# Optimization experiments

Hardware: AMD Instinct MI355X
Metric: run time of the kernel (lower is better)

The kernel has to match this reference:

```python
import jax, jax.numpy as jnp
import numpy as np
from jax import lax

A = 3          # anchors per scale
C = 80         # num foreground classes (COCO)
NMS_THRESH = 0.45
NMS_TOPK = 400
POST_NMS = 100


def setup_inputs() -> dict:
    key = jax.random.key(0)
    k0, k1, k2 = jax.random.split(key, 3)
    B = 8
    ch = A * (C + 5)  # 255
    # raw head outputs (pre-decode conv activations), modest scale so exp() stays sane
    tip0 = jax.random.normal(k0, (B, ch, 19, 19), jnp.float32) * 0.5
    tip1 = jax.random.normal(k1, (B, ch, 38, 38), jnp.float32) * 0.5
    tip2 = jax.random.normal(k2, (B, ch, 76, 76), jnp.float32) * 0.5
    # standard YOLOv3 COCO anchors, deepest scale (stride 32) first
    anchors0 = jnp.array([[116., 90.], [156., 198.], [373., 326.]], jnp.float32)
    anchors1 = jnp.array([[30., 61.], [62., 45.], [59., 119.]], jnp.float32)
    anchors2 = jnp.array([[10., 13.], [16., 30.], [33., 23.]], jnp.float32)
    return dict(tip0=tip0, tip1=tip1, tip2=tip2,
                anchors0=anchors0, anchors1=anchors1, anchors2=anchors2)


def _decode(tip, anchors, stride):
    """YOLOOutputV3 inference decode. tip: (B, A*(C+5), H, W)."""
    B, _, H, W = tip.shape
    # (B, A*(C+5), H*W) -> (B, H*W, A, C+5)
    pred = tip.reshape(B, A * (C + 5), H * W).transpose(0, 2, 1).reshape(B, H * W, A, C + 5)
    gx, gy = jnp.meshgrid(jnp.arange(W), jnp.arange(H))       # each (H, W)
    offsets = jnp.stack([gx, gy], -1).reshape(1, H * W, 1, 2).astype(tip.dtype)
    centers = (jax.nn.sigmoid(pred[..., :2]) + offsets) * stride          # (B,HW,A,2)
    scales = jnp.exp(pred[..., 2:4]) * anchors.reshape(1, 1, A, 2)        # (B,HW,A,2)
    conf = jax.nn.sigmoid(pred[..., 4:5])                                 # objectness
    cls_scores = jax.nn.sigmoid(pred[..., 5:]) * conf                      # (B,HW,A,C)
    wh = scales * 0.5
    bbox = jnp.concatenate([centers - wh, centers + wh], -1)               # corner format
    return bbox.reshape(B, H * W * A, 4), cls_scores.reshape(B, H * W * A, C)


def _pairwise_iou(b):
    """b: (K,4) corner boxes -> (K,K) IoU."""
    x1, y1, x2, y2 = b[:, 0], b[:, 1], b[:, 2], b[:, 3]
    area = jnp.maximum(x2 - x1, 0.) * jnp.maximum(y2 - y1, 0.)
    iw = jnp.maximum(jnp.minimum(x2[:, None], x2[None, :]) - jnp.maximum(x1[:, None], x1[None, :]), 0.)
    ih = jnp.maximum(jnp.minimum(y2[:, None], y2[None, :]) - jnp.maximum(y1[:, None], y1[None, :]), 0.)
    inter = iw * ih
    return inter / (area[:, None] + area[None, :] - inter + 1e-12)


def _nms_single(det):
    """Class-aware greedy NMS on one image. det: (M,6) = (cid, score, x1,y1,x2,y2)."""
    K = NMS_TOPK
    _, idx = lax.top_k(det[:, 1], K)     # sort by score, keep top K
    d = det[idx]                          # (K,6), descending score
    iou = _pairwise_iou(d[:, 2:6])
    same = d[:, 0][:, None] == d[:, 0][None, :]   # only same class suppresses
    valid = d[:, 1] > 0.
    rng = jnp.arange(K)

    def body(i, keep):
        sup = (iou[i] > NMS_THRESH) & same[i] & (rng > i) & keep[i] & valid[i]
        return keep & ~sup

    keep = lax.fori_loop(0, K, body, jnp.ones((K,), bool)) & valid
    d = jnp.where(keep[:, None], d, jnp.full_like(d, -1.))
    order = jnp.argsort(-d[:, 1])         # kept (sorted) first, suppressed (-1) last
    return d[order][:POST_NMS]            # (POST_NMS, 6)


def _detect(tip0, tip1, tip2, anchors0, anchors1, anchors2):
    dets = []
    for tip, anc, stride in ((tip0, anchors0, 32), (tip1, anchors1, 16), (tip2, anchors2, 8)):
        bbox, scores = _decode(tip, anc, stride)          # (B,N,4), (B,N,C)
        B, N, _ = bbox.shape
        ids = jnp.broadcast_to(jnp.arange(C, dtype=bbox.dtype)[None, None, :, None], (B, N, C, 1))
        sc = scores[..., None]                            # (B,N,C,1)
        bx = jnp.broadcast_to(bbox[:, :, None, :], (B, N, C, 4))
        dets.append(jnp.concatenate([ids, sc, bx], -1).reshape(B, N * C, 6))
    det = jnp.concatenate(dets, 1)                        # (B, M, 6)
    return jax.vmap(_nms_single)(det)                     # (B, POST_NMS, 6)


def reference(tip0, tip1, tip2, anchors0, anchors1, anchors2):
    res = _detect(tip0, tip1, tip2, anchors0, anchors1, anchors2)
    ids = res[..., 0:1]
    scores = res[..., 1:2]
    bboxes = res[..., 2:6]
    return ids, scores, bboxes
```

## Files before the change

### kernel.cpp

```cpp
#include <hip/hip_runtime.h>
#include <stdint.h>

#define NUMA 3
#define NUMC 80
#define CAP  49152
#define KTOP 400
#define POST 100
#define EQCAP 1024
#define PFCAP 2048
#define KEY0 0x3EE66666u
#define KEYTOP 0x3F800000u
#define LBUF 1024
#define NMASK (KTOP * 7)

typedef float f32x4 __attribute__((ext_vector_type(4)));

__device__ __forceinline__ float sigmoidf_(float x) { return 1.0f / (1.0f + expf(-x)); }
__device__ __forceinline__ unsigned uminu(unsigned a, unsigned b) { return a < b ? a : b; }

__global__ void init_kernel(unsigned* __restrict__ p) {
    int i = blockIdx.x * blockDim.x + threadIdx.x;
    if (i < 24) p[i] = 0;
}

__global__ __launch_bounds__(256) void score_main(
        const float* __restrict__ t0, const float* __restrict__ t1,
        const float* __restrict__ t2,
        unsigned* __restrict__ ccnt, unsigned* __restrict__ ckey,
        unsigned* __restrict__ cidx)
{
    __shared__ unsigned lkey[LBUF], lidx[LBUF];
    __shared__ unsigned lcnt, lbase;
    const int tid = threadIdx.x;
    if (tid == 0) lcnt = 0;
    __syncthreads();

    const int ba = blockIdx.z;
    const int b = ba / 3, a = ba - 3 * b;
    const int c0 = blockIdx.y * 10;
    const int cx = blockIdx.x;

    #define LEMIT(SC, IDX) do { \
        unsigned key_ = __float_as_uint(SC); \
        if (key_ >= KEY0) { \
            unsigned pos_ = atomicAdd(&lcnt, 1u); \
            if (pos_ < LBUF) { lkey[pos_] = key_; lidx[pos_] = (IDX); } \
        } \
    } while (0)

    if (cx < 2) {
        const int hw = cx * 256 + tid;
        if (hw < 361) {
            const float* base = t0 + (size_t)(b * 255 + a * 85) * 361;
            float cr = base[4 * 361 + hw];
            const float* p0 = base + (size_t)(5 + c0) * 361 + hw;
            float x0 = p0[0 * 361], x1 = p0[1 * 361], x2 = p0[2 * 361], x3 = p0[3 * 361];
            float x4 = p0[4 * 361], x5 = p0[5 * 361], x6 = p0[6 * 361], x7 = p0[7 * 361];
            float x8 = p0[8 * 361], x9 = p0[9 * 361];
            float cf = sigmoidf_(cr);
            unsigned ib = (unsigned)((hw * NUMA + a) * NUMC + c0);
            LEMIT(sigmoidf_(x0) * cf, ib + 0);
            LEMIT(sigmoidf_(x1) * cf, ib + 1);
            LEMIT(sigmoidf_(x2) * cf, ib + 2);
            LEMIT(sigmoidf_(x3) * cf, ib + 3);
            LEMIT(sigmoidf_(x4) * cf, ib + 4);
            LEMIT(sigmoidf_(x5) * cf, ib + 5);
            LEMIT(sigmoidf_(x6) * cf, ib + 6);
            LEMIT(sigmoidf_(x7) * cf, ib + 7);
            LEMIT(sigmoidf_(x8) * cf, ib + 8);
            LEMIT(sigmoidf_(x9) * cf, ib + 9);
        }
    } else {
        const float* tip; int vHW, v, candOff;
        if (cx < 4) { tip = t1; vHW = 361;  v = (cx - 2) * 256 + tid; candOff = 86640; }
        else        { tip = t2; vHW = 1444; v = (cx - 4) * 256 + tid; candOff = 433200; }
        if (v < vHW) {
            const f32x4* bp = (const f32x4*)(tip + (size_t)(b * 255 + a * 85) * (size_t)(vHW * 4));
            f32x4 cv = bp[(size_t)4 * vHW + v];
            const f32x4* p0 = bp + (size_t)(5 + c0) * vHW + v;
            f32x4 s0 = p0[0 * (size_t)vHW], s1 = p0[1 * (size_t)vHW];
            f32x4 s2 = p0[2 * (size_t)vHW], s3 = p0[3 * (size_t)vHW];
            f32x4 s4 = p0[4 * (size_t)vHW], s5 = p0[5 * (size_t)vHW];
            f32x4 s6 = p0[6 * (size_t)vHW], s7 = p0[7 * (size_t)vHW];
            f32x4 s8 = p0[8 * (size_t)vHW], s9 = p0[9 * (size_t)vHW];
            float cf0 = sigmoidf_(cv[0]), cf1 = sigmoidf_(cv[1]);
            float cf2 = sigmoidf_(cv[2]), cf3 = sigmoidf_(cv[3]);
            unsigned ib0 = (unsigned)(candOff + (v * 4 * NUMA + a) * NUMC + c0);
            #define EMIT4(S, U) do { \
                unsigned ib = ib0 + (U); \
                LEMIT(sigmoidf_((S)[0]) * cf0, ib); \
                LEMIT(sigmoidf_((S)[1]) * cf1, ib + 240); \
                LEMIT(sigmoidf_((S)[2]) * cf2, ib + 480); \
                LEMIT(sigmoidf_((S)[3]) * cf3, ib + 720); \
            } while (0)
            EMIT4(s0, 0); EMIT4(s1, 1); EMIT4(s2, 2); EMIT4(s3, 3);
            EMIT4(s4, 4); EMIT4(s5, 5); EMIT4(s6, 6); EMIT4(s7, 7);
            EMIT4(s8, 8); EMIT4(s9, 9);
            #undef EMIT4
        }
    }
    #undef LEMIT

    __syncthreads();
    if (tid == 0) {
        unsigned c = lcnt;
        if (c > LBUF) {
            atomicOr(&ccnt[b], 0x80000000u);
            lbase = 0xFFFFFFFFu;
        } else {
            lbase = atomicAdd(&ccnt[b], c);
        }
    }
    __syncthreads();
    unsigned c = uminu(lcnt, (unsigned)LBUF);
    unsigned basep = lbase;
    if (basep != 0xFFFFFFFFu) {
        for (unsigned i = tid; i < c; i += 256) {
            unsigned p = basep + i;
            if (p < CAP) {
                ckey[(size_t)b * CAP + p] = lkey[i];
                cidx[(size_t)b * CAP + p] = lidx[i];
            }
        }
    }
}

__device__ __forceinline__ void wave_select(const unsigned* h, int nbins, unsigned rank,
                                            unsigned* resv, int tid)
{
    if (tid >= 64) return;
    const int lane = tid;
    const int cs = nbins >> 6;
    unsigned v = 0;
    for (int k = 0; k < cs; k++) {
        int off = (k + lane) & (cs - 1);
        v += h[lane * cs + off];
    }
    unsigned S = v;
    #pragma unroll
    for (int o = 1; o < 64; o <<= 1) {
        unsigned t = (unsigned)__shfl_down((int)S, o);
        if (lane + o < 64) S += t;
    }
    unsigned long long bm = __ballot(S >= rank);
    if (bm == 0ull) bm = 1ull;
    int C = 63 - __builtin_clzll(bm);
    unsigned SC = (unsigned)__builtin_amdgcn_readlane((int)S, C);
    unsigned vC = (unsigned)__builtin_amdgcn_readlane((int)v, C);
    unsigned rem = rank - (SC - vC);
    unsigned w = (lane < cs) ? h[C * cs + lane] : 0u;
    unsigned T = w;
    #pragma unroll
    for (int o = 1; o < 64; o <<= 1) {
        unsigned t = (unsigned)__shfl_down((int)T, o);
        if (lane + o < 64) T += t;
    }
    unsigned long long bm2 = __ballot((T >= rem) && (lane < cs));
    if (bm2 == 0ull) bm2 = 1ull;
    int B = 63 - __builtin_clzll(bm2);
    unsigned TB = (unsigned)__builtin_amdgcn_readlane((int)T, B);
    unsigned wB = (unsigned)__builtin_amdgcn_readlane((int)w, B);
    if (lane == 0) {
        resv[0] = (unsigned)(C * cs + B);
        resv[1] = rem - (TB - wB);
    }
}

__global__ __launch_bounds__(1024) void fb_all(
        const float* __restrict__ t0, const float* __restrict__ t1,
        const float* __restrict__ t2,
        unsigned* __restrict__ cutb, unsigned* __restrict__ ccnt,
        unsigned* __restrict__ flags,
        unsigned* __restrict__ ckey, unsigned* __restrict__ cidx)
{
    const int b = blockIdx.x;
    unsigned cc = ccnt[b];
    if (cc >= KTOP && cc <= CAP) return;

    __shared__ unsigned lh[2048];
    __shared__ unsigned resv[2];
    __shared__ unsigned fcnt;
    const int tid = threadIdx.x;
    const int NPOS = 3 * (361 + 1444 + 5776);

    for (int i = tid; i < 2048; i += 1024) lh[i] = 0;
    if (tid == 0) fcnt = 0;
    __syncthreads();

    for (int p = tid; p < NPOS; p += 1024) {
        const float* tip; int HW, pp;
        if (p < 1083)      { tip = t0; HW = 361;  pp = p; }
        else if (p < 5415) { tip = t1; HW = 1444; pp = p - 1083; }
        else               { tip = t2; HW = 5776; pp = p - 5415; }
        int a = pp / HW, hwl = pp - a * HW;
        const float* base = tip + (size_t)(b * 255 + a * 85) * HW;
        float cf = sigmoidf_(base[4 * HW + hwl]);
        for (int u = 0; u < NUMC; u++) {
            float sc = sigmoidf_(base[(size_t)(5 + u) * HW + hwl]) * cf;
            atomicAdd(&lh[__float_as_uint(sc) >> 19], 1u);
        }
    }
    __syncthreads();
    wave_select(lh, 2048, KTOP, resv, tid);
    __syncthreads();
    unsigned cutbin = resv[0];
    unsigned cutkey = cutbin << 19;
    __syncthreads();

    unsigned* ck = ckey + (size_t)b * CAP;
    unsigned* ci = cidx + (size_t)b * CAP;
    for (int p = tid; p < NPOS; p += 1024) {
        const float* tip; int HW, pp, candOff;
        if (p < 1083)      { tip = t0; HW = 361;  pp = p;        candOff = 0; }
        else if (p < 5415) { tip = t1; HW = 1444; pp = p - 1083; candOff = 86640; }
        else               { tip = t2; HW = 5776; pp = p - 5415; candOff = 433200; }
        int a = pp / HW, hwl = pp - a * HW;
        const float* base = tip + (size_t)(b * 255 + a * 85) * HW;
        float cf = sigmoidf_(base[4 * HW + hwl]);
        unsigned ib0 = (unsigned)(candOff + (hwl * NUMA + a) * NUMC);
        for (int u = 0; u < NUMC; u++) {
            float sc = sigmoidf_(base[(size_t)(5 + u) * HW + hwl]) * cf;
            unsigned key = __float_as_uint(sc);
            if (key >= cutkey) {
                unsigned pos = atomicAdd(&fcnt, 1u);
                if (pos < CAP) { ck[pos] = key; ci[pos] = ib0 + (unsigned)u; }
            }
        }
    }
    __syncthreads();
    if (tid == 0) { ccnt[b] = fcnt; cutb[b] = cutbin; flags[b] = 1u; }
}

__global__ __launch_bounds__(1024) void topk_nms(
        const float* __restrict__ t0, const float* __restrict__ t1,
        const float* __restrict__ t2,
        const float* __restrict__ anc0, const float* __restrict__ anc1,
        const float* __restrict__ anc2,
        const unsigned* __restrict__ ckey, const unsigned* __restrict__ cidx,
        const unsigned* __restrict__ ccnt, const unsigned* __restrict__ cutb,
        const unsigned* __restrict__ flags, float* __restrict__ out)
{
    const int b = blockIdx.x;
    const int tid = threadIdx.x;
    const int T = 1024;

    __shared__ unsigned long long poolq[4160];
    unsigned* hist = (unsigned*)poolq;
    unsigned* pk   = (unsigned*)poolq + 4096;
    unsigned* pi   = (unsigned*)poolq + 6144;
    unsigned long long* maskL = poolq;
    float* bx1 = (float*)(poolq + 2800);
    float* by1 = bx1 + 400;
    float* bx2 = by1 + 400;
    float* by2 = bx2 + 400;
    int*   bcid = (int*)(poolq + 3600);
    unsigned long long* vkeep = poolq + 3800;
    float* oid = (float*)(poolq + 3808);
    float* osc = oid + 100;
    float* obb = osc + 100;

    __shared__ unsigned selk[512], seli[512];
    __shared__ unsigned eqi[EQCAP];
    __shared__ unsigned resv[2];
    __shared__ unsigned cnts[3];

    const unsigned* ck = ckey + (size_t)b * CAP;
    const unsigned* ci = cidx + (size_t)b * CAP;
    unsigned n = uminu(ccnt[b], (unsigned)CAP);

    unsigned kbase = flags[b] ? (cutb[b] << 19) : KEY0;
    unsigned span = (KEYTOP - kbase) + 1u;
    unsigned SH = 0;
    while ((span >> SH) > 2047u) SH++;

    for (int i = tid; i < 2048; i += T) hist[i] = 0;
    __syncthreads();
    {
        unsigned n4 = n >> 2;
        const uint4* ck4 = (const uint4*)ck;
        for (unsigned i = tid; i < n4; i += T) {
            uint4 k = ck4[i];
            atomicAdd(&hist[(k.x - kbase) >> SH], 1u);
            atomicAdd(&hist[(k.y - kbase) >> SH], 1u);
            atomicAdd(&hist[(k.z - kbase) >> SH], 1u);
            atomicAdd(&hist[(k.w - kbase) >> SH], 1u);
        }
        for (unsigned i = (n4 << 2) + tid; i < n; i += T)
            atomicAdd(&hist[(ck[i] - kbase) >> SH], 1u);
    }
    __syncthreads();
    wave_select(hist, 2048, KTOP, resv, tid);
    __syncthreads();
    unsigned Bf = resv[0];
    __syncthreads();

    if (tid == 0) { cnts[0] = 0; cnts[1] = 0; cnts[2] = 0; }
    __syncthreads();
    for (unsigned i = tid; i < n; i += T) {
        unsigned k = ck[i];
        if (((k - kbase) >> SH) >= Bf) {
            unsigned q = atomicAdd(&cnts[2], 1u);
            if (q < (unsigned)PFCAP) { pk[q] = k; pi[q] = ci[i]; }
        }
    }
    __syncthreads();
    unsigned pfCnt = cnts[2];
    bool useP = (pfCnt <= (unsigned)PFCAP);
    unsigned m = useP ? pfCnt : n;

    for (int i = tid; i < 4096; i += T) hist[i] = 0;
    __syncthreads();
    for (unsigned i = tid; i < m; i += T) {
        unsigned k = useP ? pk[i] : ck[i];
        atomicAdd(&hist[k >> 19], 1u);
    }
    __syncthreads();
    wave_select(hist, 4096, KTOP, resv, tid);
    __syncthreads();
    unsigned b1 = resv[0], r2 = resv[1];
    __syncthreads();

    for (int i = tid; i < 4096; i += T) hist[i] = 0;
    __syncthreads();
    for (unsigned i = tid; i < m; i += T) {
        unsigned k = useP ? pk[i] : ck[i];
        if ((k >> 19) == b1) atomicAdd(&hist[(k >> 7) & 0xFFFu], 1u);
    }
    __syncthreads();
    wave_select(hist, 4096, r2, resv, tid);
    __syncthreads();
    unsigned b2 = resv[0], r3 = resv[1];
    __syncthreads();

    for (int i = tid; i < 128; i += T) hist[i] = 0;
    __syncthreads();
    unsigned pref = (b1 << 12) | b2;
    for (unsigned i = tid; i < m; i += T) {
        unsigned k = useP ? pk[i] : ck[i];
        if ((k >> 7) == pref) atomicAdd(&hist[k & 127u], 1u);
    }
    __syncthreads();
    wave_select(hist, 128, r3, resv, tid);
    __syncthreads();
    unsigned b3 = resv[0], needEq = resv[1];
    unsigned K400 = (b1 << 19) | (b2 << 7) | b3;
    __syncthreads();

    for (int i = tid; i < 512; i += T) { selk[i] = 0u; seli[i] = 0xFFFFFFFFu; }
    for (int i = tid; i < EQCAP; i += T) eqi[i] = 0xFFFFFFFFu;
    __syncthreads();
    for (unsigned i = tid; i < m; i += T) {
        unsigned k = useP ? pk[i] : ck[i];
        if (k > K400) {
            unsigned idx = useP ? pi[i] : ci[i];
            unsigned p = atomicAdd(&cnts[0], 1u);
            if (p < 512u) { selk[p] = k; seli[p] = idx; }
        } else if (k == K400) {
            unsigned idx = useP ? pi[i] : ci[i];
            unsigned q = atomicAdd(&cnts[1], 1u);
            if (q < (unsigned)EQCAP) eqi[q] = idx;
        }
    }
    __syncthreads();
    unsigned selCnt = uminu(cnts[0], (unsigned)KTOP);
    unsigned eqN   = uminu(cnts[1], (unsigned)EQCAP);

    if (eqN > needEq) {
        int P2 = 1; while ((unsigned)P2 < eqN) P2 <<= 1;
        for (int k2 = 2; k2 <= P2; k2 <<= 1) {
            for (int j = k2 >> 1; j > 0; j >>= 1) {
                __syncthreads();
                for (int i = tid; i < P2; i += T) {
                    int ixj = i ^ j;
                    if (ixj > i && ixj < P2) {
                        unsigned va = eqi[i], vb = eqi[ixj];
                        bool up = ((i & k2) == 0);
                        if (up ? (va > vb) : (va < vb)) { eqi[i] = vb; eqi[ixj] = va; }
                    }
                }
            }
        }
        __syncthreads();
    }
    for (unsigned t2v = tid; t2v < needEq; t2v += T) {
        unsigned p = selCnt + t2v;
        if (p < KTOP) { selk[p] = K400; seli[p] = eqi[t2v]; }
    }
    __syncthreads();

    for (int k2 = 2; k2 <= 512; k2 <<= 1) {
        int j = k2 >> 1;
        for (; j >= 64; j >>= 1) {
            __syncthreads();
            if (tid < 512) {
                int i = tid, ixj = i ^ j;
                if (ixj > i) {
                    unsigned ka = selk[i], kb = selk[ixj], ia = seli[i], ib = seli[ixj];
                    bool before = (ka > kb) || (ka == kb && ia < ib);
                    bool up = ((i & k2) == 0);
                    if (up ? !before : before) {
                        selk[i] = kb; selk[ixj] = ka; seli[i] = ib; seli[ixj] = ia;
                    }
                }
            }
        }
        __syncthreads();
        if (tid < 512) {
            for (; j > 0; j >>= 1) {
                int i = tid, ixj = i ^ j;
                if (ixj > i) {
                    unsigned ka = selk[i], kb = selk[ixj], ia = seli[i], ib = seli[ixj];
                    bool before = (ka > kb) || (ka == kb && ia < ib);
                    bool up = ((i & k2) == 0);
                    if (up ? !before : before) {
                        selk[i] = kb; selk[ixj] = ka; seli[i] = ib; seli[ixj] = ia;
                    }
                }
            }
        }
    }
    __syncthreads();

    if (tid < KTOP) {
        unsigned idx = seli[tid];
        if (idx == 0xFFFFFFFFu) {
            bx1[tid] = -1.f; by1[tid] = -1.f; bx2[tid] = -1.f; by2[tid] = -1.f;
            bcid[tid] = 0;
        } else {
            const float* tip; const float* anc; int HW, W, candOff; float strideF;
            if (idx < 86640u)       { tip = t0; anc = anc0; HW = 361;  W = 19; strideF = 32.f; candOff = 0; }
            else if (idx < 433200u) { tip = t1; anc = anc1; HW = 1444; W = 38; strideF = 16.f; candOff = 86640; }
            else                    { tip = t2; anc = anc2; HW = 5776; W = 76; strideF = 8.f;  candOff = 433200; }
            unsigned local = idx - (unsigned)candOff;
            int cls = (int)(local % NUMC);
            int nn  = (int)(local / NUMC);
            int a = nn % NUMA, hwl = nn / NUMA;
            const float* base = tip + (size_t)(b * 255 + a * 85) * HW + hwl;
            float tx = base[0];
            float ty = base[(size_t)HW];
            float tw = base[(size_t)2 * HW];
            float th = base[(size_t)3 * HW];
            float fx = (float)(hwl % W), fy = (float)(hwl / W);
            float cx = (sigmoidf_(tx) + fx) * strideF;
            float cy = (sigmoidf_(ty) + fy) * strideF;
            float hw_ = expf(tw) * anc[2 * a]     * 0.5f;
            float hh_ = expf(th) * anc[2 * a + 1] * 0.5f;
            bx1[tid] = cx - hw_; by1[tid] = cy - hh_;
            bx2[tid] = cx + hw_; by2[tid] = cy + hh_;
            bcid[tid] = cls;
        }
    }
    __syncthreads();

    for (int p = tid; p < NMASK; p += T) {
        int i = p / 7, w = p - i * 7;
        float x1i = bx1[i], y1i = by1[i], x2i = bx2[i], y2i = by2[i];
        float ai = fmaxf(x2i - x1i, 0.f) * fmaxf(y2i - y1i, 0.f);
        int cidI = bcid[i];
        unsigned long long mq = 0ull;
        int j0 = w * 64;
        int j1 = j0 + 64; if (j1 > KTOP) j1 = KTOP;
        int js = j0 > i + 1 ? j0 : i + 1;
        for (int j = js; j < j1; j++) {
            if (bcid[j] != cidI) continue;
            float iw = fminf(x2i, bx2[j]) - fmaxf(x1i, bx1[j]);
            float ih = fminf(y2i, by2[j]) - fmaxf(y1i, by1[j]);
            iw = fmaxf(iw, 0.f); ih = fmaxf(ih, 0.f);
            float inter = iw * ih;
            float aj = fmaxf(bx2[j] - bx1[j], 0.f) * fmaxf(by2[j] - by1[j], 0.f);
            float iou = inter / (ai + aj - inter + 1e-12f);
            if (iou > 0.45f) mq |= (1ull << (j - j0));
        }
        maskL[p] = mq;
    }
    __syncthreads();

    if (tid < 64) {
        const int lane = tid;
        unsigned long long keep = 0ull;
        if (lane < 7) keep = (lane == 6) ? 0xFFFFull : ~0ull;
        unsigned long long mb[8];
        #pragma unroll
        for (int k = 0; k < 8; k++)
            mb[k] = (lane < 7) ? maskL[k * 7 + lane] : 0ull;
        for (int ib = 0; ib < KTOP; ib += 8) {
            #pragma unroll
            for (int k = 0; k < 8; k++) {
                int i = ib + k;
                unsigned long long mq = mb[k];
                int nf = ib + 8 + k;
                mb[k] = (lane < 7 && nf < KTOP) ? maskL[nf * 7 + lane] : 0ull;
                int w = i >> 6;
                unsigned klo = (unsigned)__builtin_amdgcn_readlane((int)(unsigned)(keep & 0xFFFFFFFFull), w);
                unsigned khi = (unsigned)__builtin_amdgcn_readlane((int)(unsigned)(keep >> 32), w);
                unsigned long long kw = ((unsigned long long)khi << 32) | klo;
                if ((kw >> (i & 63)) & 1ull) keep &= ~mq;
            }
        }
        if (lane < 7) vkeep[lane] = keep;
    } else {
        int q = tid - 64;
        if (q < POST) { oid[q] = -1.f; osc[q] = -1.f; }
        if (q < POST * 4) obb[q] = -1.f;
    }
    __syncthreads();

    if (tid < KTOP) {
        int w = tid >> 6, bp = tid & 63;
        unsigned long long kw = vkeep[w];
        if ((kw >> bp) & 1ull) {
            int r = 0;
            for (int q = 0; q < w; q++) r += __popcll(vkeep[q]);
            r += __popcll(kw & ((1ull << bp) - 1ull));
            if (r < POST) {
                oid[r] = (float)bcid[tid];
                osc[r] = __uint_as_float(selk[tid]);
                obb[r * 4 + 0] = bx1[tid];
                obb[r * 4 + 1] = by1[tid];
                obb[r * 4 + 2] = bx2[tid];
                obb[r * 4 + 3] = by2[tid];
            }
        }
    }
    __syncthreads();
    if (tid < POST) {
        out[b * POST + tid]       = oid[tid];
        out[800 + b * POST + tid] = osc[tid];
    }
    if (tid < POST * 4) out[1600 + b * POST * 4 + tid] = obb[tid];
}

extern "C" void kernel_launch(void* const* d_in, const int* in_sizes, int n_in,
                              void* d_out, int out_size, void* d_ws, size_t ws_size,
                              hipStream_t stream)
{
    const float* tip0 = (const float*)d_in[0];
    const float* tip1 = (const float*)d_in[1];
    const float* tip2 = (const float*)d_in[2];
    const float* anc0 = (const float*)d_in[3];
    const float* anc1 = (const float*)d_in[4];
    const float* anc2 = (const float*)d_in[5];
    float* out = (float*)d_out;

    unsigned* cutb  = (unsigned*)d_ws;
    unsigned* ccnt  = cutb + 8;
    unsigned* flags = ccnt + 8;
    unsigned* ckey  = flags + 8;
    unsigned* cidx  = ckey + (size_t)8 * CAP;

    init_kernel<<<1, 64, 0, stream>>>(cutb);

    dim3 g(10, 8, 24);
    score_main<<<g, 256, 0, stream>>>(tip0, tip1, tip2, ccnt, ckey, cidx);
    fb_all<<<8, 1024, 0, stream>>>(tip0, tip1, tip2, cutb, ccnt, flags, ckey, cidx);
    topk_nms<<<8, 1024, 0, stream>>>(tip0, tip1, tip2, anc0, anc1, anc2,
                                     ckey, cidx, ccnt, cutb, flags, out);
}
```

Before: 198.9 us.

## Split top-k/NMS into select, parallel mask, and greedy kernels; prefilter logits

The monolithic per-batch topk_nms kernel is split into three kernels. topk_sel decodes boxes to global memory, mask_kernel computes the IoU masks across many blocks per batch, and greedy_kernel runs the serial suppression scan. The mask loop also rotates the j start per word to spread shared-memory accesses. Separately, score_main now compares raw logits against a threshold derived from objectness, so the sigmoid is skipped for candidates that cannot pass. The cost is two extra launches and round trips through global memory.

After: 191.3 us. 3.8% less time.

```diff
diff --git a/kernel.cpp b/kernel.cpp
--- a/kernel.cpp
+++ b/kernel.cpp
@@ -18,6 +18,13 @@
 __device__ __forceinline__ float sigmoidf_(float x) { return 1.0f / (1.0f + expf(-x)); }
 __device__ __forceinline__ unsigned uminu(unsigned a, unsigned b) { return a < b ? a : b; }
 
+__device__ __forceinline__ float thr_for(float cf) {
+    if (!(cf >= 0.45f)) return 3.0e38f;
+    float q = 0.449f / cf;
+    float r = q / (1.0f - q);
+    return logf(r) - 0.01f;
+}
+
 __global__ void init_kernel(unsigned* __restrict__ p) {
     int i = blockIdx.x * blockDim.x + threadIdx.x;
     if (i < 24) p[i] = 0;
@@ -58,17 +65,18 @@
             float x4 = p0[4 * 361], x5 = p0[5 * 361], x6 = p0[6 * 361], x7 = p0[7 * 361];
             float x8 = p0[8 * 361], x9 = p0[9 * 361];
             float cf = sigmoidf_(cr);
+            float xt = thr_for(cf);
             unsigned ib = (unsigned)((hw * NUMA + a) * NUMC + c0);
-            LEMIT(sigmoidf_(x0) * cf, ib + 0);
-            LEMIT(sigmoidf_(x1) * cf, ib + 1);
-            LEMIT(sigmoidf_(x2) * cf, ib + 2);
-            LEMIT(sigmoidf_(x3) * cf, ib + 3);
-            LEMIT(sigmoidf_(x4) * cf, ib + 4);
-            LEMIT(sigmoidf_(x5) * cf, ib + 5);
-            LEMIT(sigmoidf_(x6) * cf, ib + 6);
-            LEMIT(sigmoidf_(x7) * cf, ib + 7);
-            LEMIT(sigmoidf_(x8) * cf, ib + 8);
-            LEMIT(sigmoidf_(x9) * cf, ib + 9);
+            if (x0 > xt) LEMIT(sigmoidf_(x0) * cf, ib + 0);
+            if (x1 > xt) LEMIT(sigmoidf_(x1) * cf, ib + 1);
+            if (x2 > xt) LEMIT(sigmoidf_(x2) * cf, ib + 2);
+            if (x3 > xt) LEMIT(sigmoidf_(x3) * cf, ib + 3);
+            if (x4 > xt) LEMIT(sigmoidf_(x4) * cf, ib + 4);
+            if (x5 > xt) LEMIT(sigmoidf_(x5) * cf, ib + 5);
+            if (x6 > xt) LEMIT(sigmoidf_(x6) * cf, ib + 6);
+            if (x7 > xt) LEMIT(sigmoidf_(x7) * cf, ib + 7);
+            if (x8 > xt) LEMIT(sigmoidf_(x8) * cf, ib + 8);
+            if (x9 > xt) LEMIT(sigmoidf_(x9) * cf, ib + 9);
         }
     } else {
         const float* tip; int vHW, v, candOff;
@@ -85,13 +93,15 @@
             f32x4 s8 = p0[8 * (size_t)vHW], s9 = p0[9 * (size_t)vHW];
             float cf0 = sigmoidf_(cv[0]), cf1 = sigmoidf_(cv[1]);
             float cf2 = sigmoidf_(cv[2]), cf3 = sigmoidf_(cv[3]);
+            float xt0 = thr_for(cf0), xt1 = thr_for(cf1);
+            float xt2 = thr_for(cf2), xt3 = thr_for(cf3);
             unsigned ib0 = (unsigned)(candOff + (v * 4 * NUMA + a) * NUMC + c0);
             #define EMIT4(S, U) do { \
                 unsigned ib = ib0 + (U); \
-                LEMIT(sigmoidf_((S)[0]) * cf0, ib); \
-                LEMIT(sigmoidf_((S)[1]) * cf1, ib + 240); \
-                LEMIT(sigmoidf_((S)[2]) * cf2, ib + 480); \
-                LEMIT(sigmoidf_((S)[3]) * cf3, ib + 720); \
+                if ((S)[0] > xt0) LEMIT(sigmoidf_((S)[0]) * cf0, ib); \
+                if ((S)[1] > xt1) LEMIT(sigmoidf_((S)[1]) * cf1, ib + 240); \
+                if ((S)[2] > xt2) LEMIT(sigmoidf_((S)[2]) * cf2, ib + 480); \
+                if ((S)[3] > xt3) LEMIT(sigmoidf_((S)[3]) * cf3, ib + 720); \
             } while (0)
             EMIT4(s0, 0); EMIT4(s1, 1); EMIT4(s2, 2); EMIT4(s3, 3);
             EMIT4(s4, 4); EMIT4(s5, 5); EMIT4(s6, 6); EMIT4(s7, 7);
@@ -231,37 +241,27 @@
     if (tid == 0) { ccnt[b] = fcnt; cutb[b] = cutbin; flags[b] = 1u; }
 }
 
-__global__ __launch_bounds__(1024) void topk_nms(
+__global__ __launch_bounds__(1024) void topk_sel(
         const float* __restrict__ t0, const float* __restrict__ t1,
         const float* __restrict__ t2,
         const float* __restrict__ anc0, const float* __restrict__ anc1,
         const float* __restrict__ anc2,
         const unsigned* __restrict__ ckey, const unsigned* __restrict__ cidx,
         const unsigned* __restrict__ ccnt, const unsigned* __restrict__ cutb,
-        const unsigned* __restrict__ flags, float* __restrict__ out)
+        const unsigned* __restrict__ flags,
+        float* __restrict__ dX1, float* __restrict__ dY1,
+        float* __restrict__ dX2, float* __restrict__ dY2,
+        float* __restrict__ dSC, unsigned* __restrict__ dCID)
 {
     const int b = blockIdx.x;
     const int tid = threadIdx.x;
     const int T = 1024;
 
-    __shared__ unsigned long long poolq[4160];
-    unsigned* hist = (unsigned*)poolq;
-    unsigned* pk   = (unsigned*)poolq + 4096;
-    unsigned* pi   = (unsigned*)poolq + 6144;
-    unsigned long long* maskL = poolq;
-    float* bx1 = (float*)(poolq + 2800);
-    float* by1 = bx1 + 400;
-    float* bx2 = by1 + 400;
-    float* by2 = bx2 + 400;
-    int*   bcid = (int*)(poolq + 3600);
-    unsigned long long* vkeep = poolq + 3800;
-    float* oid = (float*)(poolq + 3808);
-    float* osc = oid + 100;
-    float* obb = osc + 100;
-
+    __shared__ unsigned hist[4096];
+    __shared__ unsigned resv[2];
     __shared__ unsigned selk[512], seli[512];
     __shared__ unsigned eqi[EQCAP];
-    __shared__ unsigned resv[2];
+    __shared__ unsigned pk[PFCAP], pi[PFCAP];
     __shared__ unsigned cnts[3];
 
     const unsigned* ck = ckey + (size_t)b * CAP;
@@ -423,9 +423,10 @@
 
     if (tid < KTOP) {
         unsigned idx = seli[tid];
+        int o = b * KTOP + tid;
         if (idx == 0xFFFFFFFFu) {
-            bx1[tid] = -1.f; by1[tid] = -1.f; bx2[tid] = -1.f; by2[tid] = -1.f;
-            bcid[tid] = 0;
+            dX1[o] = -1.f; dY1[o] = -1.f; dX2[o] = -1.f; dY2[o] = -1.f;
+            dSC[o] = __uint_as_float(selk[tid]); dCID[o] = 0u;
         } else {
             const float* tip; const float* anc; int HW, W, candOff; float strideF;
             if (idx < 86640u)       { tip = t0; anc = anc0; HW = 361;  W = 19; strideF = 32.f; candOff = 0; }
@@ -445,34 +446,70 @@
             float cy = (sigmoidf_(ty) + fy) * strideF;
             float hw_ = expf(tw) * anc[2 * a]     * 0.5f;
             float hh_ = expf(th) * anc[2 * a + 1] * 0.5f;
-            bx1[tid] = cx - hw_; by1[tid] = cy - hh_;
-            bx2[tid] = cx + hw_; by2[tid] = cy + hh_;
-            bcid[tid] = cls;
-        }
-    }
-    __syncthreads();
-
-    for (int p = tid; p < NMASK; p += T) {
+            dX1[o] = cx - hw_; dY1[o] = cy - hh_;
+            dX2[o] = cx + hw_; dY2[o] = cy + hh_;
+            dSC[o] = __uint_as_float(selk[tid]);
+            dCID[o] = (unsigned)cls;
+        }
+    }
+}
+
+__global__ __launch_bounds__(256) void mask_kernel(
+        const float* __restrict__ dX1, const float* __restrict__ dY1,
+        const float* __restrict__ dX2, const float* __restrict__ dY2,
+        const unsigned* __restrict__ dCID, unsigned long long* __restrict__ maskG)
+{
+    __shared__ float lx1[KTOP], ly1[KTOP], lx2[KTOP], ly2[KTOP];
+    __shared__ int lcid[KTOP];
+    const int b = blockIdx.y;
+    const int tid = threadIdx.x;
+    for (int i = tid; i < KTOP; i += 256) {
+        int o = b * KTOP + i;
+        lx1[i] = dX1[o]; ly1[i] = dY1[o];
+        lx2[i] = dX2[o]; ly2[i] = dY2[o];
+        lcid[i] = (int)dCID[o];
+    }
+    __syncthreads();
+    int p = blockIdx.x * 256 + tid;
+    if (p < NMASK) {
         int i = p / 7, w = p - i * 7;
-        float x1i = bx1[i], y1i = by1[i], x2i = bx2[i], y2i = by2[i];
+        float x1i = lx1[i], y1i = ly1[i], x2i = lx2[i], y2i = ly2[i];
         float ai = fmaxf(x2i - x1i, 0.f) * fmaxf(y2i - y1i, 0.f);
-        int cidI = bcid[i];
-        unsigned long long mq = 0ull;
+        int cidI = lcid[i];
+        unsigned long long m = 0ull;
         int j0 = w * 64;
-        int j1 = j0 + 64; if (j1 > KTOP) j1 = KTOP;
-        int js = j0 > i + 1 ? j0 : i + 1;
-        for (int j = js; j < j1; j++) {
-            if (bcid[j] != cidI) continue;
-            float iw = fminf(x2i, bx2[j]) - fmaxf(x1i, bx1[j]);
-            float ih = fminf(y2i, by2[j]) - fmaxf(y1i, by1[j]);
+        int rot = (9 * w) & 63;
+        for (int t = 0; t < 64; t++) {
+            int j = j0 + ((t + rot) & 63);
+            if (j >= KTOP || j <= i) continue;
+            if (lcid[j] != cidI) continue;
+            float iw = fminf(x2i, lx2[j]) - fmaxf(x1i, lx1[j]);
+            float ih = fminf(y2i, ly2[j]) - fmaxf(y1i, ly1[j]);
             iw = fmaxf(iw, 0.f); ih = fmaxf(ih, 0.f);
             float inter = iw * ih;
-            float aj = fmaxf(bx2[j] - bx1[j], 0.f) * fmaxf(by2[j] - by1[j], 0.f);
+            float aj = fmaxf(lx2[j] - lx1[j], 0.f) * fmaxf(ly2[j] - ly1[j], 0.f);
             float iou = inter / (ai + aj - inter + 1e-12f);
-            if (iou > 0.45f) mq |= (1ull << (j - j0));
-        }
-        maskL[p] = mq;
-    }
+            if (iou > 0.45f) m |= (1ull << (j - j0));
+        }
+        maskG[(size_t)b * NMASK + p] = m;
+    }
+}
+
+__global__ __launch_bounds__(512) void greedy_kernel(
+        const float* __restrict__ dX1, const float* __restrict__ dY1,
+        const float* __restrict__ dX2, const float* __restrict__ dY2,
+        const float* __restrict__ dSC, const unsigned* __restrict__ dCID,
+        const unsigned long long* __restrict__ maskG, float* __restrict__ out)
+{
+    __shared__ unsigned long long maskL[NMASK];
+    __shared__ unsigned long long vkeep[7];
+    __shared__ float oid[POST], osc[POST], obb[POST * 4];
+    const int b = blockIdx.x;
+    const int tid = threadIdx.x;
+
+    for (int i = tid; i < NMASK; i += 512) maskL[i] = maskG[(size_t)b * NMASK + i];
+    if (tid < POST) { oid[tid] = -1.f; osc[tid] = -1.f; }
+    if (tid < POST * 4) obb[tid] = -1.f;
     __syncthreads();
 
     if (tid < 64) {
@@ -487,21 +524,17 @@
             #pragma unroll
             for (int k = 0; k < 8; k++) {
                 int i = ib + k;
-                unsigned long long mq = mb[k];
+                unsigned long long m = mb[k];
                 int nf = ib + 8 + k;
                 mb[k] = (lane < 7 && nf < KTOP) ? maskL[nf * 7 + lane] : 0ull;
                 int w = i >> 6;
                 unsigned klo = (unsigned)__builtin_amdgcn_readlane((int)(unsigned)(keep & 0xFFFFFFFFull), w);
                 unsigned khi = (unsigned)__builtin_amdgcn_readlane((int)(unsigned)(keep >> 32), w);
                 unsigned long long kw = ((unsigned long long)khi << 32) | klo;
-                if ((kw >> (i & 63)) & 1ull) keep &= ~mq;
+                if ((kw >> (i & 63)) & 1ull) keep &= ~m;
             }
         }
         if (lane < 7) vkeep[lane] = keep;
-    } else {
-        int q = tid - 64;
-        if (q < POST) { oid[q] = -1.f; osc[q] = -1.f; }
-        if (q < POST * 4) obb[q] = -1.f;
     }
     __syncthreads();
 
@@ -513,12 +546,13 @@
             for (int q = 0; q < w; q++) r += __popcll(vkeep[q]);
             r += __popcll(kw & ((1ull << bp) - 1ull));
             if (r < POST) {
-                oid[r] = (float)bcid[tid];
-                osc[r] = __uint_as_float(selk[tid]);
-                obb[r * 4 + 0] = bx1[tid];
-                obb[r * 4 + 1] = by1[tid];
-                obb[r * 4 + 2] = bx2[tid];
-                obb[r * 4 + 3] = by2[tid];
+                int o = b * KTOP + tid;
+                oid[r] = (float)(int)dCID[o];
+                osc[r] = dSC[o];
+                obb[r * 4 + 0] = dX1[o];
+                obb[r * 4 + 1] = dY1[o];
+                obb[r * 4 + 2] = dX2[o];
+                obb[r * 4 + 3] = dY2[o];
             }
         }
     }
@@ -547,12 +581,23 @@
     unsigned* flags = ccnt + 8;
     unsigned* ckey  = flags + 8;
     unsigned* cidx  = ckey + (size_t)8 * CAP;
+    float*    dX1   = (float*)(cidx + (size_t)8 * CAP);
+    float*    dY1   = dX1 + 8 * KTOP;
+    float*    dX2   = dY1 + 8 * KTOP;
+    float*    dY2   = dX2 + 8 * KTOP;
+    float*    dSC   = dY2 + 8 * KTOP;
+    unsigned* dCID  = (unsigned*)(dSC + 8 * KTOP);
+    unsigned long long* maskG = (unsigned long long*)(dCID + 8 * KTOP);
 
     init_kernel<<<1, 64, 0, stream>>>(cutb);
 
     dim3 g(10, 8, 24);
     score_main<<<g, 256, 0, stream>>>(tip0, tip1, tip2, ccnt, ckey, cidx);
     fb_all<<<8, 1024, 0, stream>>>(tip0, tip1, tip2, cutb, ccnt, flags, ckey, cidx);
-    topk_nms<<<8, 1024, 0, stream>>>(tip0, tip1, tip2, anc0, anc1, anc2,
-                                     ckey, cidx, ccnt, cutb, flags, out);
-}
+    topk_sel<<<8, 1024, 0, stream>>>(tip0, tip1, tip2, anc0, anc1, anc2,
+                                     ckey, cidx, ccnt, cutb, flags,
+                                     dX1, dY1, dX2, dY2, dSC, dCID);
+    mask_kernel<<<dim3((NMASK + 255) / 256, 8), 256, 0, stream>>>(
+        dX1, dY1, dX2, dY2, dCID, maskG);
+    greedy_kernel<<<8, 512, 0, stream>>>(dX1, dY1, dX2, dY2, dSC, dCID, maskG, out);
+}
```
